# Kernel tuning notes

Hardware: AMD Instinct MI355X
Metric: run time of the kernel (lower is better)

## Reference

```python
import jax, jax.numpy as jnp
import numpy as np

NUM_NODES = 100000
NUM_EDGES = 1600000
D = 128

def sage_conv(x, src, dst, Wl, bl, Wr):
    # PyG SAGEConv (mean aggr): out = lin_l(mean_{j->i} x_j) + lin_r(x_i)
    msgs = x[src]                                            # [E, D] gather
    agg = jax.ops.segment_sum(msgs, dst, num_segments=x.shape[0])  # [N, D]
    deg = jax.ops.segment_sum(jnp.ones((src.shape[0],), x.dtype), dst,
                              num_segments=x.shape[0])       # [N]
    mean = agg / jnp.maximum(deg, 1.0)[:, None]
    return mean @ Wl.T + bl + x @ Wr.T

def setup_inputs() -> dict:
    key = jax.random.key(0)
    ks = jax.random.split(key, 16)
    s = 1.0 / np.sqrt(D)
    inp = {
        'x': jax.random.randint(ks[0], (NUM_NODES, 1), 0, NUM_NODES),
        'edge_index': jax.random.randint(ks[1], (2, NUM_EDGES), 0, NUM_NODES),
        'batch': jnp.zeros((NUM_NODES,), dtype=jnp.int64),
        'item_emb': jax.random.normal(ks[2], (NUM_NODES, D), jnp.float32),
        'edge_emb': jax.random.normal(ks[3], (NUM_EDGES, D), jnp.float32),
        'Wl1': jax.random.uniform(ks[4], (D, D), jnp.float32, -s, s),
        'bl1': jnp.zeros((D,), jnp.float32),
        'Wr1': jax.random.uniform(ks[5], (D, D), jnp.float32, -s, s),
        'Wl2': jax.random.uniform(ks[6], (D, D), jnp.float32, -s, s),
        'bl2': jnp.zeros((D,), jnp.float32),
        'Wr2': jax.random.uniform(ks[7], (D, D), jnp.float32, -s, s),
        'Wl3': jax.random.uniform(ks[8], (D, D), jnp.float32, -s, s),
        'bl3': jnp.zeros((D,), jnp.float32),
        'Wr3': jax.random.uniform(ks[9], (D, D), jnp.float32, -s, s),
        'W_lin1': jax.random.uniform(ks[10], (D, D), jnp.float32, -s, s),
        'b_lin1': jnp.zeros((D,), jnp.float32),
        'W_lin2': jax.random.uniform(ks[11], (D, D), jnp.float32, -s, s),
        'b_lin2': jnp.zeros((D,), jnp.float32),
    }
    return inp

def reference(x, edge_index, batch, item_emb, edge_emb,
              Wl1, bl1, Wr1, Wl2, bl2, Wr2, Wl3, bl3, Wr3,
              W_lin1, b_lin1, W_lin2, b_lin2):
    src, dst = edge_index[0], edge_index[1]
    h = item_emb[x[:, 0]]                      # embedding lookup + squeeze(1) -> [N, D]
    e = edge_emb                               # edge_embedding(arange(E)) == full table
    h = jax.nn.relu(sage_conv(h, src, dst, Wl1, bl1, Wr1))
    h = jax.nn.relu(sage_conv(h, src, dst, Wl2, bl2, Wr2))
    h = jax.nn.relu(sage_conv(h, src, dst, Wl3, bl3, Wr3))
    h = jax.nn.relu(h @ W_lin1.T + b_lin1)     # dropout is identity in eval mode
    e_out = jax.nn.relu(e @ W_lin2.T + b_lin2)
    return h, e_out
```

## Files before the change

### kernel.cpp

```cpp
#include <hip/hip_runtime.h>

#define NN  100000
#define NNP 100096
#define NE  1600000
#define DD  128

typedef __attribute__((ext_vector_type(8))) short bf16x8;
typedef __attribute__((ext_vector_type(4))) float f32x4;

__device__ __forceinline__ float bf2f(unsigned short u){
  union { unsigned int i; float f; } v; v.i = ((unsigned int)u) << 16; return v.f;
}
__device__ __forceinline__ unsigned short f2bf(float f){
  union { float f; unsigned int i; } v; v.f = f;
  unsigned int u = v.i;
  return (unsigned short)((u + 0x7fffu + ((u >> 16) & 1u)) >> 16);
}
__device__ __forceinline__ unsigned int cvt_pk_bf16(float lo, float hi){
  unsigned int r;
  asm("v_cvt_pk_bf16_f32 %0, %1, %2" : "=v"(r) : "v"(lo), "v"(hi));
  return r;
}

struct WPtrs { const float* w[8]; };
__global__ __launch_bounds__(256) void cvt_w_all(WPtrs wp, unsigned short* __restrict__ o){
  int t = blockIdx.x * 256 + threadIdx.x;
  int m = t >> 13, i = t & 8191;
  float2 v = ((const float2*)wp.w[m])[i];
  ((unsigned int*)o)[t] = cvt_pk_bf16(v.x, v.y);
}

__device__ __forceinline__ void stage_mat(const unsigned short* __restrict__ Bg,
                                          unsigned short* sB){
  int t = threadIdx.x;
  #pragma unroll
  for (int it = 0; it < 8; ++it){
    int idx = it * 256 + t;
    int kc = idx >> 7, col = idx & 127;
    uint4 v = *(const uint4*)(Bg + (size_t)col * DD + kc * 8);
    *(uint4*)(sB + (size_t)idx * 8) = v;
  }
}

__device__ __forceinline__ void edge_run(const float* __restrict__ A,
    const unsigned short* __restrict__ Wg, const float* __restrict__ bias,
    float* __restrict__ out, unsigned short* sB, int tile0, int cnt)
{
  stage_mat(Wg, sB);
  __syncthreads();
  int wave = threadIdx.x >> 6, lane = threadIdx.x & 63;
  int lr = lane & 15, lk = lane >> 4;
  float bv[8];
  #pragma unroll
  for (int j = 0; j < 8; ++j) bv[j] = bias[j * 16 + lr];

  for (int t = 0; t < cnt; ++t){
    size_t r0 = (size_t)(tile0 + t) * 128 + (size_t)wave * 32;
    const float* Ap = A + (r0 + lr) * DD + lk * 8;
    bf16x8 a[2][4];
    #pragma unroll
    for (int g = 0; g < 2; ++g){
      #pragma unroll
      for (int ks = 0; ks < 4; ++ks){
        f32x4 a0 = *(const f32x4*)(Ap + (size_t)g * 16 * DD + ks * 32);
        f32x4 a1 = *(const f32x4*)(Ap + (size_t)g * 16 * DD + ks * 32 + 4);
        union { bf16x8 v; unsigned int u[4]; } au;
        au.u[0] = cvt_pk_bf16(a0[0], a0[1]);
        au.u[1] = cvt_pk_bf16(a0[2], a0[3]);
        au.u[2] = cvt_pk_bf16(a1[0], a1[1]);
        au.u[3] = cvt_pk_bf16(a1[2], a1[3]);
        a[g][ks] = au.v;
      }
    }
    f32x4 acc[2][8];
    #pragma unroll
    for (int g = 0; g < 2; ++g)
      #pragma unroll
      for (int j = 0; j < 8; ++j) acc[g][j] = (f32x4){0.f, 0.f, 0.f, 0.f};
    #pragma unroll
    for (int ks = 0; ks < 4; ++ks){
      #pragma unroll
      for (int j = 0; j < 8; ++j){
        bf16x8 b = *(const bf16x8*)(sB + ((ks * 4 + lk) * 128 + j * 16 + lr) * 8);
        acc[0][j] = __builtin_amdgcn_mfma_f32_16x16x32_bf16(a[0][ks], b, acc[0][j], 0, 0, 0);
        acc[1][j] = __builtin_amdgcn_mfma_f32_16x16x32_bf16(a[1][ks], b, acc[1][j], 0, 0, 0);
      }
    }
    #pragma unroll
    for (int g = 0; g < 2; ++g)
      #pragma unroll
      for (int j = 0; j < 8; ++j)
        #pragma unroll
        for (int r = 0; r < 4; ++r){
          size_t row = r0 + g * 16 + lk * 4 + r;
          out[row * DD + j * 16 + lr] = fmaxf(acc[g][j][r] + bv[j], 0.f);
        }
  }
}

#define EDGE_ARGS const float* __restrict__ eA, const unsigned short* __restrict__ eW, \
                  const float* __restrict__ eBias, float* __restrict__ eOut, \
                  int eTileBase, int eBlocks
#define EDGE_PASS eA, eW, eBias, eOut
#define EDGE_CHUNK 5

__global__ __launch_bounds__(256) void countdeg_edge(
    const int* __restrict__ dst, int* __restrict__ deg, int n, EDGE_ARGS){
  __shared__ unsigned short sB[16384];
  if ((int)blockIdx.x < eBlocks){
    edge_run(EDGE_PASS, sB, eTileBase + blockIdx.x * EDGE_CHUNK, EDGE_CHUNK);
    return;
  }
  int t = (blockIdx.x - eBlocks) * 256 + threadIdx.x;
  if (t < n) atomicAdd(&deg[dst[t]], 1);
}

__global__ __launch_bounds__(256) void fillcsr_edge(
    const int* __restrict__ src, const int* __restrict__ dst,
    const int* __restrict__ row_start, int* __restrict__ cursor,
    int* __restrict__ csr, int n, EDGE_ARGS){
  __shared__ unsigned short sB[16384];
  if ((int)blockIdx.x < eBlocks){
    edge_run(EDGE_PASS, sB, eTileBase + blockIdx.x * EDGE_CHUNK, EDGE_CHUNK);
    return;
  }
  int t = (blockIdx.x - eBlocks) * 256 + threadIdx.x;
  if (t < n){
    int d = dst[t];
    int pos = atomicAdd(&cursor[d], 1);
    csr[row_start[d] + pos] = src[t];
  }
}

#define SCAN_CHUNK 1024
__global__ __launch_bounds__(256) void partial_sums(const int* __restrict__ deg,
                                                    int* __restrict__ partials, int n){
  __shared__ int lds[256];
  int t = threadIdx.x;
  int base = blockIdx.x * SCAN_CHUNK + t * 4;
  int s = 0;
  #pragma unroll
  for (int i = 0; i < 4; ++i){ int idx = base + i; s += (idx < n) ? deg[idx] : 0; }
  lds[t] = s; __syncthreads();
  for (int off = 128; off > 0; off >>= 1){
    if (t < off) lds[t] += lds[t + off];
    __syncthreads();
  }
  if (t == 0) partials[blockIdx.x] = lds[0];
}

__global__ void scan_partials(int* partials, int nb){
  if (threadIdx.x == 0 && blockIdx.x == 0){
    int acc = 0;
    for (int i = 0; i < nb; ++i){ int v = partials[i]; partials[i] = acc; acc += v; }
  }
}

__global__ __launch_bounds__(256) void scan_block(const int* __restrict__ deg,
                                                  const int* __restrict__ partials,
                                                  int* __restrict__ row_start, int n){
  __shared__ int lds[256];
  int t = threadIdx.x;
  int base = blockIdx.x * SCAN_CHUNK + t * 4;
  int v[4]; int s = 0;
  #pragma unroll
  for (int i = 0; i < 4; ++i){ int idx = base + i; v[i] = (idx < n) ? deg[idx] : 0; s += v[i]; }
  lds[t] = s; __syncthreads();
  for (int off = 1; off < 256; off <<= 1){
    int x = (t >= off) ? lds[t - off] : 0;
    __syncthreads();
    lds[t] += x;
    __syncthreads();
  }
  int excl = ((t == 0) ? 0 : lds[t - 1]) + partials[blockIdx.x];
  #pragma unroll
  for (int i = 0; i < 4; ++i){ int idx = base + i; if (idx < n) row_start[idx] = excl; excl += v[i]; }
}

__global__ __launch_bounds__(256) void gather_h0(const int* __restrict__ x,
                                                 const float* __restrict__ emb,
                                                 unsigned short* __restrict__ h, int n){
  int t = blockIdx.x * 256 + threadIdx.x;
  if (t >= n * 64) return;
  int node = t >> 6, p = t & 63;
  int s = x[node];
  float2 v = *(const float2*)(emb + (size_t)s * DD + p * 2);
  ((unsigned int*)h)[t] = cvt_pk_bf16(v.x, v.y);
}

__global__ __launch_bounds__(256) void aggregate2(const unsigned short* __restrict__ h,
                                                  const int* __restrict__ csr,
                                                  const int* __restrict__ row_start,
                                                  const int* __restrict__ deg,
                                                  unsigned short* __restrict__ mean, int n){
  int node = blockIdx.x * 4 + (threadIdx.x >> 6);
  if (node >= n) return;
  int lane = threadIdx.x & 63;
  int st = row_start[node];
  int d = deg[node];
  const unsigned int* hp = (const unsigned int*)h;
  float s0 = 0.f, s1 = 0.f, t0 = 0.f, t1 = 0.f;
  float u0 = 0.f, u1 = 0.f, w0 = 0.f, w1 = 0.f;
  int i = 0;
  for (; i + 4 <= d; i += 4){
    int n0 = csr[st + i], n1 = csr[st + i + 1], n2 = csr[st + i + 2], n3 = csr[st + i + 3];
    unsigned int v0 = hp[(size_t)n0 * 64 + lane];
    unsigned int v1 = hp[(size_t)n1 * 64 + lane];
    unsigned int v2 = hp[(size_t)n2 * 64 + lane];
    unsigned int v3 = hp[(size_t)n3 * 64 + lane];
    s0 += bf2f((unsigned short)(v0 & 0xffffu)); s1 += bf2f((unsigned short)(v0 >> 16));
    t0 += bf2f((unsigned short)(v1 & 0xffffu)); t1 += bf2f((unsigned short)(v1 >> 16));
    u0 += bf2f((unsigned short)(v2 & 0xffffu)); u1 += bf2f((unsigned short)(v2 >> 16));
    w0 += bf2f((unsigned short)(v3 & 0xffffu)); w1 += bf2f((unsigned short)(v3 >> 16));
  }
  for (; i < d; ++i){
    int s = csr[st + i];
    unsigned int v = hp[(size_t)s * 64 + lane];
    s0 += bf2f((unsigned short)(v & 0xffffu)); s1 += bf2f((unsigned short)(v >> 16));
  }
  s0 += t0 + u0 + w0;
  s1 += t1 + u1 + w1;
  float inv = 1.0f / fmaxf((float)d, 1.0f);
  ((unsigned int*)mean)[(size_t)node * 64 + lane] = cvt_pk_bf16(s0 * inv, s1 * inv);
}

template<int DUAL, int OUTF32>
__global__ __launch_bounds__(256) void node_edge(
    const unsigned short* __restrict__ A1, const unsigned short* __restrict__ B1g,
    const unsigned short* __restrict__ A2, const unsigned short* __restrict__ B2g,
    const float* __restrict__ bias, void* __restrict__ outp, int M,
    EDGE_ARGS)
{
  __shared__ unsigned short sB[DUAL ? 32768 : 16384];
  if ((int)blockIdx.x < eBlocks){
    edge_run(EDGE_PASS, sB, eTileBase + blockIdx.x * EDGE_CHUNK, EDGE_CHUNK);
    return;
  }
  stage_mat(B1g, sB);
  if (DUAL) stage_mat(B2g, sB + 16384);
  __syncthreads();
  int wave = threadIdx.x >> 6, lane = threadIdx.x & 63;
  int lr = lane & 15, lk = lane >> 4;
  float bv[8];
  #pragma unroll
  for (int j = 0; j < 8; ++j) bv[j] = bias[j * 16 + lr];

  int tile = blockIdx.x - eBlocks;
  size_t r0 = (size_t)tile * 128 + wave * 32;
  f32x4 acc[2][8];
  #pragma unroll
  for (int g = 0; g < 2; ++g)
    #pragma unroll
    for (int j = 0; j < 8; ++j) acc[g][j] = (f32x4){0.f, 0.f, 0.f, 0.f};

  {
    const unsigned short* Ap = A1 + (r0 + lr) * DD + lk * 8;
    bf16x8 a[2][4];
    #pragma unroll
    for (int g = 0; g < 2; ++g)
      #pragma unroll
      for (int ks = 0; ks < 4; ++ks)
        a[g][ks] = *(const bf16x8*)(Ap + (size_t)g * 16 * DD + ks * 32);
    #pragma unroll
    for (int ks = 0; ks < 4; ++ks){
      #pragma unroll
      for (int j = 0; j < 8; ++j){
        bf16x8 b = *(const bf16x8*)(sB + ((ks * 4 + lk) * 128 + j * 16 + lr) * 8);
        acc[0][j] = __builtin_amdgcn_mfma_f32_16x16x32_bf16(a[0][ks], b, acc[0][j], 0, 0, 0);
        acc[1][j] = __builtin_amdgcn_mfma_f32_16x16x32_bf16(a[1][ks], b, acc[1][j], 0, 0, 0);
      }
    }
  }
  if (DUAL){
    const unsigned short* Ap = A2 + (r0 + lr) * DD + lk * 8;
    bf16x8 a[2][4];
    #pragma unroll
    for (int g = 0; g < 2; ++g)
      #pragma unroll
      for (int ks = 0; ks < 4; ++ks)
        a[g][ks] = *(const bf16x8*)(Ap + (size_t)g * 16 * DD + ks * 32);
    #pragma unroll
    for (int ks = 0; ks < 4; ++ks){
      #pragma unroll
      for (int j = 0; j < 8; ++j){
        bf16x8 b = *(const bf16x8*)(sB + 16384 + ((ks * 4 + lk) * 128 + j * 16 + lr) * 8);
        acc[0][j] = __builtin_amdgcn_mfma_f32_16x16x32_bf16(a[0][ks], b, acc[0][j], 0, 0, 0);
        acc[1][j] = __builtin_amdgcn_mfma_f32_16x16x32_bf16(a[1][ks], b, acc[1][j], 0, 0, 0);
      }
    }
  }
  #pragma unroll
  for (int g = 0; g < 2; ++g)
    #pragma unroll
    for (int j = 0; j < 8; ++j)
      #pragma unroll
      for (int r = 0; r < 4; ++r){
        size_t row = r0 + g * 16 + lk * 4 + r;
        float v = fmaxf(acc[g][j][r] + bv[j], 0.f);
        if (OUTF32){
          if (row < (size_t)M) ((float*)outp)[row * DD + j * 16 + lr] = v;
        } else {
          ((unsigned short*)outp)[row * DD + j * 16 + lr] = f2bf(v);
        }
      }
}

extern "C" void kernel_launch(void* const* d_in, const int* in_sizes, int n_in,
                              void* d_out, int out_size, void* d_ws, size_t ws_size,
                              hipStream_t stream)
{
  const int*   x    = (const int*)d_in[0];
  const int*   ei   = (const int*)d_in[1];
  const int*   srcp = ei;
  const int*   dstp = ei + NE;
  const float* item = (const float*)d_in[3];
  const float* eemb = (const float*)d_in[4];
  WPtrs wp;
  wp.w[0] = (const float*)d_in[5];
  wp.w[1] = (const float*)d_in[7];
  wp.w[2] = (const float*)d_in[8];
  wp.w[3] = (const float*)d_in[10];
  wp.w[4] = (const float*)d_in[11];
  wp.w[5] = (const float*)d_in[13];
  wp.w[6] = (const float*)d_in[14];
  wp.w[7] = (const float*)d_in[16];
  const float* bl1 = (const float*)d_in[6];
  const float* bl2 = (const float*)d_in[9];
  const float* bl3 = (const float*)d_in[12];
  const float* bq1 = (const float*)d_in[15];
  const float* bq2 = (const float*)d_in[17];

  char* ws = (char*)d_ws;
  size_t o = 0;
  auto alloc = [&](size_t bytes) -> void* {
    void* p = ws + o;
    o += (bytes + 255) & ~(size_t)255;
    return p;
  };
  unsigned short* wbf      = (unsigned short*)alloc(8 * 16384 * 2);
  int*            deg      = (int*)alloc((size_t)NNP * 4);
  int*            cursor   = (int*)alloc((size_t)NNP * 4);
  int*            row_st   = (int*)alloc((size_t)NNP * 4);
  int*            partials = (int*)alloc(4096);
  int*            csr      = (int*)alloc((size_t)NE * 4);
  unsigned short* mean     = (unsigned short*)alloc((size_t)NNP * DD * 2);
  unsigned short* h_a      = (unsigned short*)alloc((size_t)NNP * DD * 2);
  unsigned short* h_b      = (unsigned short*)alloc((size_t)NNP * DD * 2);

  float* out_h = (float*)d_out;
  float* out_e = out_h + (size_t)NN * DD;
  const unsigned short* eW = wbf + 7 * 16384;

  hipMemsetAsync(deg, 0, (size_t)NNP * 4 * 2, stream);

  cvt_w_all<<<256, 256, 0, stream>>>(wp, wbf);

  int eb = 0;
  const int e_cd = 250, e_fc = 250, e_nd = 500, e_fin = 500;

  const int nb = (NN + SCAN_CHUNK - 1) / SCAN_CHUNK;
  const int csr_blk = (NE + 255) / 256;

  countdeg_edge<<<e_cd + csr_blk, 256, 0, stream>>>(dstp, deg, NE,
      eemb, eW, bq2, out_e, eb * EDGE_CHUNK, e_cd); eb += e_cd;
  partial_sums<<<nb, 256, 0, stream>>>(deg, partials, NN);
  scan_partials<<<1, 64, 0, stream>>>(partials, nb);
  scan_block<<<nb, 256, 0, stream>>>(deg, partials, row_st, NN);
  fillcsr_edge<<<e_fc + csr_blk, 256, 0, stream>>>(srcp, dstp, row_st, cursor, csr, NE,
      eemb, eW, bq2, out_e, eb * EDGE_CHUNK, e_fc); eb += e_fc;

  gather_h0<<<(NN * 64 + 255) / 256, 256, 0, stream>>>(x, item, h_a, NN);

  const int agg_grid   = (NN + 3) / 4;
  const int node_tiles = NNP / 128;

  aggregate2<<<agg_grid, 256, 0, stream>>>(h_a, csr, row_st, deg, mean, NN);
  node_edge<1,0><<<e_nd + node_tiles, 256, 0, stream>>>(mean, wbf + 0*16384, h_a, wbf + 1*16384,
      bl1, h_b, NN, eemb, eW, bq2, out_e, eb * EDGE_CHUNK, e_nd); eb += e_nd;
  aggregate2<<<agg_grid, 256, 0, stream>>>(h_b, csr, row_st, deg, mean, NN);
  node_edge<1,0><<<e_nd + node_tiles, 256, 0, stream>>>(mean, wbf + 2*16384, h_b, wbf + 3*16384,
      bl2, h_a, NN, eemb, eW, bq2, out_e, eb * EDGE_CHUNK, e_nd); eb += e_nd;
  aggregate2<<<agg_grid, 256, 0, stream>>>(h_a, csr, row_st, deg, mean, NN);
  node_edge<1,0><<<e_nd + node_tiles, 256, 0, stream>>>(mean, wbf + 4*16384, h_a, wbf + 5*16384,
      bl3, h_b, NN, eemb, eW, bq2, out_e, eb * EDGE_CHUNK, e_nd); eb += e_nd;

  node_edge<0,1><<<e_fin + node_tiles, 256, 0, stream>>>(h_b, wbf + 6*16384, h_b, wbf + 6*16384,
      bq1, out_h, NN, eemb, eW, bq2, out_e, eb * EDGE_CHUNK, e_fin); eb += e_fin;
}
```

Before: 836.1 us.

## Interleave edge GEMM blocks with graph kernels and vectorize aggregation

The edge-embedding GEMM tiles move off the node GEMM kernels and into the aggregation kernels. Edge blocks are interleaved one per S blocks across countdeg, fillcsr and aggregation grids, so the compute-bound edge work overlaps the memory-bound gather and atomic phases instead of running at the front of each launch. Aggregation now uses 16-byte loads, with four lane groups each handling different neighbors and combining through shuffles, and it reads row start and degree as wave-uniform values. The tile-base offsets and block counts are hand-computed and must cover all edge tiles exactly. Any mismatch would leave outputs unwritten or written twice.

New measurement: 1.686 ms. +101.6%, slower.

```diff
diff --git a/kernel.cpp b/kernel.cpp
--- a/kernel.cpp
+++ b/kernel.cpp
@@ -104,27 +104,30 @@
 #define EDGE_PASS eA, eW, eBias, eOut
 #define EDGE_CHUNK 5
 
+
 __global__ __launch_bounds__(256) void countdeg_edge(
-    const int* __restrict__ dst, int* __restrict__ deg, int n, EDGE_ARGS){
+    const int* __restrict__ dst, int* __restrict__ deg, int n, int S, EDGE_ARGS){
   __shared__ unsigned short sB[16384];
-  if ((int)blockIdx.x < eBlocks){
-    edge_run(EDGE_PASS, sB, eTileBase + blockIdx.x * EDGE_CHUNK, EDGE_CHUNK);
+  int grp = blockIdx.x / S, r = blockIdx.x % S;
+  if (r == S - 1){
+    if (grp < eBlocks) edge_run(EDGE_PASS, sB, eTileBase + grp * EDGE_CHUNK, EDGE_CHUNK);
     return;
   }
-  int t = (blockIdx.x - eBlocks) * 256 + threadIdx.x;
+  int t = (blockIdx.x - grp) * 256 + threadIdx.x;
   if (t < n) atomicAdd(&deg[dst[t]], 1);
 }
 
 __global__ __launch_bounds__(256) void fillcsr_edge(
     const int* __restrict__ src, const int* __restrict__ dst,
     const int* __restrict__ row_start, int* __restrict__ cursor,
-    int* __restrict__ csr, int n, EDGE_ARGS){
+    int* __restrict__ csr, int n, int S, EDGE_ARGS){
   __shared__ unsigned short sB[16384];
-  if ((int)blockIdx.x < eBlocks){
-    edge_run(EDGE_PASS, sB, eTileBase + blockIdx.x * EDGE_CHUNK, EDGE_CHUNK);
+  int grp = blockIdx.x / S, r = blockIdx.x % S;
+  if (r == S - 1){
+    if (grp < eBlocks) edge_run(EDGE_PASS, sB, eTileBase + grp * EDGE_CHUNK, EDGE_CHUNK);
     return;
   }
-  int t = (blockIdx.x - eBlocks) * 256 + threadIdx.x;
+  int t = (blockIdx.x - grp) * 256 + threadIdx.x;
   if (t < n){
     int d = dst[t];
     int pos = atomicAdd(&cursor[d], 1);
@@ -188,54 +191,80 @@
   ((unsigned int*)h)[t] = cvt_pk_bf16(v.x, v.y);
 }
 
-__global__ __launch_bounds__(256) void aggregate2(const unsigned short* __restrict__ h,
-                                                  const int* __restrict__ csr,
-                                                  const int* __restrict__ row_start,
-                                                  const int* __restrict__ deg,
-                                                  unsigned short* __restrict__ mean, int n){
-  int node = blockIdx.x * 4 + (threadIdx.x >> 6);
+__device__ __forceinline__ void add8(float* a, uint4 v){
+  a[0] += bf2f((unsigned short)(v.x & 0xffffu)); a[1] += bf2f((unsigned short)(v.x >> 16));
+  a[2] += bf2f((unsigned short)(v.y & 0xffffu)); a[3] += bf2f((unsigned short)(v.y >> 16));
+  a[4] += bf2f((unsigned short)(v.z & 0xffffu)); a[5] += bf2f((unsigned short)(v.z >> 16));
+  a[6] += bf2f((unsigned short)(v.w & 0xffffu)); a[7] += bf2f((unsigned short)(v.w >> 16));
+}
+
+__global__ __launch_bounds__(256) void agg_edge(
+    const unsigned short* __restrict__ h,
+    const int* __restrict__ csr, const int* __restrict__ row_start,
+    const int* __restrict__ deg, unsigned short* __restrict__ mean, int n,
+    int S, EDGE_ARGS)
+{
+  __shared__ unsigned short sB[16384];
+  int grp = blockIdx.x / S, r = blockIdx.x % S;
+  if (r == S - 1){
+    if (grp < eBlocks) edge_run(EDGE_PASS, sB, eTileBase + grp * EDGE_CHUNK, EDGE_CHUNK);
+    return;
+  }
+  int hostIdx = blockIdx.x - grp;
+  int node = hostIdx * 4 + (threadIdx.x >> 6);
   if (node >= n) return;
   int lane = threadIdx.x & 63;
-  int st = row_start[node];
-  int d = deg[node];
-  const unsigned int* hp = (const unsigned int*)h;
-  float s0 = 0.f, s1 = 0.f, t0 = 0.f, t1 = 0.f;
-  float u0 = 0.f, u1 = 0.f, w0 = 0.f, w1 = 0.f;
-  int i = 0;
-  for (; i + 4 <= d; i += 4){
-    int n0 = csr[st + i], n1 = csr[st + i + 1], n2 = csr[st + i + 2], n3 = csr[st + i + 3];
-    unsigned int v0 = hp[(size_t)n0 * 64 + lane];
-    unsigned int v1 = hp[(size_t)n1 * 64 + lane];
-    unsigned int v2 = hp[(size_t)n2 * 64 + lane];
-    unsigned int v3 = hp[(size_t)n3 * 64 + lane];
-    s0 += bf2f((unsigned short)(v0 & 0xffffu)); s1 += bf2f((unsigned short)(v0 >> 16));
-    t0 += bf2f((unsigned short)(v1 & 0xffffu)); t1 += bf2f((unsigned short)(v1 >> 16));
-    u0 += bf2f((unsigned short)(v2 & 0xffffu)); u1 += bf2f((unsigned short)(v2 >> 16));
-    w0 += bf2f((unsigned short)(v3 & 0xffffu)); w1 += bf2f((unsigned short)(v3 >> 16));
-  }
-  for (; i < d; ++i){
-    int s = csr[st + i];
-    unsigned int v = hp[(size_t)s * 64 + lane];
-    s0 += bf2f((unsigned short)(v & 0xffffu)); s1 += bf2f((unsigned short)(v >> 16));
-  }
-  s0 += t0 + u0 + w0;
-  s1 += t1 + u1 + w1;
-  float inv = 1.0f / fmaxf((float)d, 1.0f);
-  ((unsigned int*)mean)[(size_t)node * 64 + lane] = cvt_pk_bf16(s0 * inv, s1 * inv);
+  int g = lane >> 4, c = lane & 15;
+  int st = __builtin_amdgcn_readfirstlane(row_start[node]);
+  int d  = __builtin_amdgcn_readfirstlane(deg[node]);
+  const uint4* hp4 = (const uint4*)h;
+  float acc[8];
+  #pragma unroll
+  for (int j = 0; j < 8; ++j) acc[j] = 0.f;
+
+  if (d > 0){
+    int k = 0;
+    for (; k + 8 <= d; k += 8){
+      int s0 = csr[st + k + g];
+      int s1 = csr[st + k + 4 + g];
+      uint4 v0 = hp4[(size_t)s0 * 16 + c];
+      uint4 v1 = hp4[(size_t)s1 * 16 + c];
+      add8(acc, v0);
+      add8(acc, v1);
+    }
+    if (k < d){
+      int i0 = k + g, i1 = k + 4 + g;
+      int s0 = csr[st + min(i0, d - 1)];
+      int s1 = csr[st + min(i1, d - 1)];
+      uint4 v0 = hp4[(size_t)s0 * 16 + c];
+      uint4 v1 = hp4[(size_t)s1 * 16 + c];
+      if (i0 < d) add8(acc, v0);
+      if (i1 < d) add8(acc, v1);
+    }
+    #pragma unroll
+    for (int j = 0; j < 8; ++j){
+      acc[j] += __shfl_xor(acc[j], 16, 64);
+      acc[j] += __shfl_xor(acc[j], 32, 64);
+    }
+  }
+  if (g == 0){
+    float inv = 1.0f / fmaxf((float)d, 1.0f);
+    uint4 o;
+    o.x = cvt_pk_bf16(acc[0] * inv, acc[1] * inv);
+    o.y = cvt_pk_bf16(acc[2] * inv, acc[3] * inv);
+    o.z = cvt_pk_bf16(acc[4] * inv, acc[5] * inv);
+    o.w = cvt_pk_bf16(acc[6] * inv, acc[7] * inv);
+    ((uint4*)mean)[(size_t)node * 16 + c] = o;
+  }
 }
 
 template<int DUAL, int OUTF32>
-__global__ __launch_bounds__(256) void node_edge(
+__global__ __launch_bounds__(256) void gemm_node3(
     const unsigned short* __restrict__ A1, const unsigned short* __restrict__ B1g,
     const unsigned short* __restrict__ A2, const unsigned short* __restrict__ B2g,
-    const float* __restrict__ bias, void* __restrict__ outp, int M,
-    EDGE_ARGS)
+    const float* __restrict__ bias, void* __restrict__ outp, int M)
 {
   __shared__ unsigned short sB[DUAL ? 32768 : 16384];
-  if ((int)blockIdx.x < eBlocks){
-    edge_run(EDGE_PASS, sB, eTileBase + blockIdx.x * EDGE_CHUNK, EDGE_CHUNK);
-    return;
-  }
   stage_mat(B1g, sB);
   if (DUAL) stage_mat(B2g, sB + 16384);
   __syncthreads();
@@ -245,8 +274,7 @@
   #pragma unroll
   for (int j = 0; j < 8; ++j) bv[j] = bias[j * 16 + lr];
 
-  int tile = blockIdx.x - eBlocks;
-  size_t r0 = (size_t)tile * 128 + wave * 32;
+  size_t r0 = (size_t)blockIdx.x * 128 + wave * 32;
   f32x4 acc[2][8];
   #pragma unroll
   for (int g = 0; g < 2; ++g)
@@ -355,35 +383,29 @@
 
   cvt_w_all<<<256, 256, 0, stream>>>(wp, wbf);
 
-  int eb = 0;
-  const int e_cd = 250, e_fc = 250, e_nd = 500, e_fin = 500;
-
   const int nb = (NN + SCAN_CHUNK - 1) / SCAN_CHUNK;
-  const int csr_blk = (NE + 255) / 256;
-
-  countdeg_edge<<<e_cd + csr_blk, 256, 0, stream>>>(dstp, deg, NE,
-      eemb, eW, bq2, out_e, eb * EDGE_CHUNK, e_cd); eb += e_cd;
+
+  countdeg_edge<<<6600, 256, 0, stream>>>(dstp, deg, NE, 33,
+      eemb, eW, bq2, out_e, 0, 200);
   partial_sums<<<nb, 256, 0, stream>>>(deg, partials, NN);
   scan_partials<<<1, 64, 0, stream>>>(partials, nb);
   scan_block<<<nb, 256, 0, stream>>>(deg, partials, row_st, NN);
-  fillcsr_edge<<<e_fc + csr_blk, 256, 0, stream>>>(srcp, dstp, row_st, cursor, csr, NE,
-      eemb, eW, bq2, out_e, eb * EDGE_CHUNK, e_fc); eb += e_fc;
+  fillcsr_edge<<<6510, 256, 0, stream>>>(srcp, dstp, row_st, cursor, csr, NE, 42,
+      eemb, eW, bq2, out_e, 1000, 155);
 
   gather_h0<<<(NN * 64 + 255) / 256, 256, 0, stream>>>(x, item, h_a, NN);
 
-  const int agg_grid   = (NN + 3) / 4;
   const int node_tiles = NNP / 128;
 
-  aggregate2<<<agg_grid, 256, 0, stream>>>(h_a, csr, row_st, deg, mean, NN);
-  node_edge<1,0><<<e_nd + node_tiles, 256, 0, stream>>>(mean, wbf + 0*16384, h_a, wbf + 1*16384,
-      bl1, h_b, NN, eemb, eW, bq2, out_e, eb * EDGE_CHUNK, e_nd); eb += e_nd;
-  aggregate2<<<agg_grid, 256, 0, stream>>>(h_b, csr, row_st, deg, mean, NN);
-  node_edge<1,0><<<e_nd + node_tiles, 256, 0, stream>>>(mean, wbf + 2*16384, h_b, wbf + 3*16384,
-      bl2, h_a, NN, eemb, eW, bq2, out_e, eb * EDGE_CHUNK, e_nd); eb += e_nd;
-  aggregate2<<<agg_grid, 256, 0, stream>>>(h_a, csr, row_st, deg, mean, NN);
-  node_edge<1,0><<<e_nd + node_tiles, 256, 0, stream>>>(mean, wbf + 4*16384, h_a, wbf + 5*16384,
-      bl3, h_b, NN, eemb, eW, bq2, out_e, eb * EDGE_CHUNK, e_nd); eb += e_nd;
-
-  node_edge<0,1><<<e_fin + node_tiles, 256, 0, stream>>>(h_b, wbf + 6*16384, h_b, wbf + 6*16384,
-      bq1, out_h, NN, eemb, eW, bq2, out_e, eb * EDGE_CHUNK, e_fin); eb += e_fin;
-}
+  agg_edge<<<25740, 256, 0, stream>>>(h_a, csr, row_st, deg, mean, NN, 36,
+      eemb, eW, bq2, out_e, 1775, 715);
+  gemm_node3<1,0><<<node_tiles, 256, 0, stream>>>(mean, wbf + 0*16384, h_a, wbf + 1*16384, bl1, h_b, NN);
+  agg_edge<<<25740, 256, 0, stream>>>(h_b, csr, row_st, deg, mean, NN, 36,
+      eemb, eW, bq2, out_e, 5350, 715);
+  gemm_node3<1,0><<<node_tiles, 256, 0, stream>>>(mean, wbf + 2*16384, h_b, wbf + 3*16384, bl2, h_a, NN);
+  agg_edge<<<25740, 256, 0, stream>>>(h_a, csr, row_st, deg, mean, NN, 36,
+      eemb, eW, bq2, out_e, 8925, 715);
+  gemm_node3<1,0><<<node_tiles, 256, 0, stream>>>(mean, wbf + 4*16384, h_a, wbf + 5*16384, bl3, h_b, NN);
+
+  gemm_node3<0,1><<<node_tiles, 256, 0, stream>>>(h_b, wbf + 6*16384, h_b, wbf + 6*16384, bq1, out_h, NN);
+}
```
